# Performance work log

Measured on AMD Instinct MI355X. Metric: run time of the kernel, lower is better.

The kernel has to match this reference:

```python
import jax, jax.numpy as jnp
import numpy as np

V, E, H, S = 50257, 1024, 1024, 2048


def setup_inputs() -> dict:
    key = jax.random.key(0)
    ks = jax.random.split(key, 24)
    def n(k, shape, s=0.02):
        return jax.random.normal(k, shape, dtype=jnp.float32) * s
    inp = {
        "x": jax.random.normal(ks[0], (1, E), dtype=jnp.float32),
        "encoder_outputs": jax.random.normal(ks[1], (S, 2 * H), dtype=jnp.float32),
        "sentence": jax.random.randint(ks[2], (S,), 0, V, dtype=jnp.int32).at[0].set(7),
        "prev_probs": jax.random.uniform(ks[3], (V + S,), dtype=jnp.float32),
        "h0": n(ks[4], (1, H), 1.0),
        "c0": n(ks[5], (1, H), 1.0),
        "attn_W": n(ks[6], (S, 2 * H)), "attn_b": jnp.zeros((S,), jnp.float32),
        "comb_W": n(ks[7], (H, 2 * H)), "comb_b": jnp.zeros((H,), jnp.float32),
        "Ws_W": n(ks[8], (H, 2 * H)), "Ws_b": jnp.zeros((H,), jnp.float32),
        "Wo_W": n(ks[9], (V, H)), "Wo_b": jnp.zeros((V,), jnp.float32),
        "Wc_W": n(ks[10], (H, 2 * H)), "Wc_b": jnp.zeros((H,), jnp.float32),
        "W_ih": n(ks[11], (4 * H, E + 2 * H)), "W_hh": n(ks[12], (4 * H, H)),
        "b_ih": jnp.zeros((4 * H,), jnp.float32), "b_hh": jnp.zeros((4 * H,), jnp.float32),
        "prev_word": 7,
    }
    return inp


def reference(x, encoder_outputs, sentence, prev_probs, h0, c0,
              attn_W, attn_b, comb_W, comb_b, Ws_W, Ws_b,
              Wo_W, Wo_b, Wc_W, Wc_b, W_ih, W_hh, b_ih, b_hh, prev_word):
    xe, h, c = x[0], h0[0], c0[0]            # [E], [H], [H]
    # attentive read: attention over encoder positions, then combine to [H]
    att_logits = jnp.concatenate([xe, h]) @ attn_W.T + attn_b      # [S]
    attn_w = jax.nn.softmax(att_logits)
    ctx = attn_w @ encoder_outputs                                 # [2H]
    attentive = ctx @ comb_W.T + comb_b                            # [H]
    # selective read (copy mechanism): positions where sentence == prev_word
    probs_c = prev_probs[V:]                                       # [S]
    rho = jnp.where(sentence == prev_word, probs_c, 0.0)
    rho = rho / (rho.sum() + 1e-9)
    selective = (rho @ encoder_outputs) @ Ws_W.T + Ws_b            # [H]
    # single LSTM step (PyTorch gate order i,f,g,o)
    lstm_in = jnp.concatenate([xe, selective, attentive])          # [E+2H]
    gates = lstm_in @ W_ih.T + b_ih + h @ W_hh.T + b_hh            # [4H]
    i, f, g, o = jnp.split(gates, 4)
    c1 = jax.nn.sigmoid(f) * c + jax.nn.sigmoid(i) * jnp.tanh(g)
    h1 = jax.nn.sigmoid(o) * jnp.tanh(c1)                          # [H]
    # generate + copy scores, joint softmax
    score_g = h1 @ Wo_W.T + Wo_b                                   # [V]
    score_c = jnp.tanh(encoder_outputs @ Wc_W.T + Wc_b) @ h1       # [S]
    probs = jax.nn.softmax(jnp.concatenate([score_g, score_c]))    # [V+S]
    return probs, h1[None, :], c1[None, :]
```

## Files before the change

### kernel.cpp

```cpp
#include <hip/hip_runtime.h>
#include <hip/hip_bf16.h>
#include <math.h>

#define VV 50257
#define EE 1024
#define HH 1024
#define SS 2048
#define VS (VV + SS)

#define NSCB 2048

#define OFF_LOGA   0
#define OFF_CTX    2048
#define OFF_SEL    4096
#define OFF_LSTMIN 6144
#define OFF_GATES  9216
#define OFF_LOG    13312
#define OFF_MS     65664
#define OFF_LS     67712
#define OFF_T0     69760
#define OFF_T1     (69760 + 2048*1024)
#define OFF_ENCB   (OFF_T1 + 2048*1024)
#define OFF_WCB    (OFF_ENCB + 2048*1024)

typedef __attribute__((ext_vector_type(8))) short bf16x8;
typedef __attribute__((ext_vector_type(8))) unsigned short u16x8;
typedef __attribute__((ext_vector_type(4))) float f32x4;

__device__ inline float wave_reduce(float v) {
    #pragma unroll
    for (int off = 32; off > 0; off >>= 1) v += __shfl_down(v, off, 64);
    return v;
}

__device__ inline unsigned short f2bf(float f) {
    unsigned int u = __builtin_bit_cast(unsigned int, f);
    u += 0x7FFFu + ((u >> 16) & 1u);
    return (unsigned short)(u >> 16);
}

__global__ __launch_bounds__(256) void k_front(
        const float* __restrict__ x, const float* __restrict__ h0,
        const float* __restrict__ attn_W, const float* __restrict__ attn_b,
        float* __restrict__ loga,
        const float* __restrict__ enc, const float* __restrict__ Wc_W,
        unsigned short* __restrict__ encb, unsigned short* __restrict__ Wcb,
        float* __restrict__ ctxsel, float* __restrict__ lstm_in) {
    int bx = blockIdx.x, tid = threadIdx.x;
    if (bx < 512) {
        int wave = (bx * 256 + tid) >> 6;
        int lane = tid & 63;
        const float4* rp = (const float4*)(attn_W + (size_t)wave * 2048);
        float acc = 0.f;
        #pragma unroll
        for (int k = 0; k < 8; ++k) {
            int idx = lane + 64 * k;
            float4 w = rp[idx];
            int j = idx * 4;
            const float* cat = (j < 1024) ? (x + j) : (h0 + (j - 1024));
            acc += w.x * cat[0] + w.y * cat[1] + w.z * cat[2] + w.w * cat[3];
        }
        acc = wave_reduce(acc);
        if (lane == 0) loga[wave] = acc + attn_b[wave];
        return;
    }
    if (bx < 1280) {
        bool isenc = bx < 1024;
        int b = isenc ? bx - 512 : bx - 1024;
        const float* src = isenc ? enc : Wc_W;
        unsigned short* dst = isenc ? encb : Wcb;
        size_t base = (size_t)b * 8192;
        #pragma unroll
        for (int p = 0; p < 8; ++p) {
            size_t idx = base + p * 1024 + tid * 4;
            float4 v = *(const float4*)(src + idx);
            ushort4 o = { f2bf(v.x), f2bf(v.y), f2bf(v.z), f2bf(v.w) };
            *(ushort4*)(dst + idx) = o;
        }
        return;
    }
    if (bx == 1280) {
        for (int j = tid; j < 4096; j += 256) ctxsel[j] = 0.f;
        return;
    }
    for (int j = tid; j < EE; j += 256) lstm_in[j] = x[j];
}

__global__ __launch_bounds__(256) void k_ctx(
        const float* __restrict__ enc, const float* __restrict__ logits,
        const int* __restrict__ sentence, const float* __restrict__ prev_probs,
        const int* __restrict__ prev_word,
        float* __restrict__ ctx, float* __restrict__ selctx) {
    __shared__ float red[256];
    __shared__ float aw[64], rh[64];
    int tid = threadIdx.x;
    float m = -1e30f;
    for (int s = tid; s < SS; s += 256) m = fmaxf(m, logits[s]);
    red[tid] = m; __syncthreads();
    for (int o = 128; o > 0; o >>= 1) { if (tid < o) red[tid] = fmaxf(red[tid], red[tid + o]); __syncthreads(); }
    m = red[0]; __syncthreads();
    float sum = 0.f;
    for (int s = tid; s < SS; s += 256) sum += __expf(logits[s] - m);
    red[tid] = sum; __syncthreads();
    for (int o = 128; o > 0; o >>= 1) { if (tid < o) red[tid] += red[tid + o]; __syncthreads(); }
    float inv = 1.f / red[0]; __syncthreads();
    int pw = prev_word[0];
    float rsum = 0.f;
    for (int s = tid; s < SS; s += 256) rsum += (sentence[s] == pw) ? prev_probs[VV + s] : 0.f;
    red[tid] = rsum; __syncthreads();
    for (int o = 128; o > 0; o >>= 1) { if (tid < o) red[tid] += red[tid + o]; __syncthreads(); }
    float rinv = 1.f / (red[0] + 1e-9f); __syncthreads();
    int s0 = blockIdx.y * 64;
    if (tid < 64) {
        int s = s0 + tid;
        aw[tid] = __expf(logits[s] - m) * inv;
        rh[tid] = ((sentence[s] == pw) ? prev_probs[VV + s] : 0.f) * rinv;
    }
    __syncthreads();
    int col4 = blockIdx.x * 256 + tid;
    float4 a = {0.f, 0.f, 0.f, 0.f}, r = {0.f, 0.f, 0.f, 0.f};
    const float4* p = (const float4*)enc + (size_t)s0 * 512 + col4;
    #pragma unroll 4
    for (int i = 0; i < 64; ++i) {
        float4 v = p[(size_t)i * 512];
        float w = aw[i], q = rh[i];
        a.x += w * v.x; a.y += w * v.y; a.z += w * v.z; a.w += w * v.w;
        r.x += q * v.x; r.y += q * v.y; r.z += q * v.z; r.w += q * v.w;
    }
    int c = col4 * 4;
    atomicAdd(&ctx[c], a.x); atomicAdd(&ctx[c+1], a.y); atomicAdd(&ctx[c+2], a.z); atomicAdd(&ctx[c+3], a.w);
    atomicAdd(&selctx[c], r.x); atomicAdd(&selctx[c+1], r.y); atomicAdd(&selctx[c+2], r.z); atomicAdd(&selctx[c+3], r.w);
}

__global__ __launch_bounds__(256) void k_comb(
        const float* __restrict__ ctx, const float* __restrict__ selctx,
        const float* __restrict__ comb_W, const float* __restrict__ comb_b,
        const float* __restrict__ Ws_W, const float* __restrict__ Ws_b,
        float* __restrict__ lstm_in) {
    int wave = (blockIdx.x * blockDim.x + threadIdx.x) >> 6;
    int lane = threadIdx.x & 63;
    bool sel = wave >= 1024;
    int i = sel ? wave - 1024 : wave;
    const float4* rp = (const float4*)((sel ? Ws_W : comb_W) + (size_t)i * 2048);
    const float4* vp = (const float4*)(sel ? selctx : ctx);
    float acc = 0.f;
    #pragma unroll
    for (int k = 0; k < 8; ++k) {
        int idx = lane + 64 * k;
        float4 w = rp[idx]; float4 v = vp[idx];
        acc += w.x * v.x + w.y * v.y + w.z * v.z + w.w * v.w;
    }
    acc = wave_reduce(acc);
    if (lane == 0) lstm_in[sel ? (1024 + i) : (2048 + i)] = acc + (sel ? Ws_b[i] : comb_b[i]);
}

__global__ __launch_bounds__(256) void k_gates_gemm(
        const float* __restrict__ lstm_in, const float* __restrict__ h0,
        const float* __restrict__ W_ih, const float* __restrict__ W_hh,
        const float* __restrict__ b_ih, const float* __restrict__ b_hh,
        float* __restrict__ gates,
        const unsigned short* __restrict__ Ab,
        const unsigned short* __restrict__ Bb,
        float* __restrict__ T0, float* __restrict__ T1) {
    __shared__ __attribute__((aligned(16))) unsigned short As[128 * 32];
    __shared__ __attribute__((aligned(16))) unsigned short Bs[128 * 32];
    int tid = threadIdx.x;
    if (blockIdx.x < 1024) {
        int wave = (blockIdx.x * 256 + tid) >> 6;
        int lane = tid & 63;
        const float4* rp = (const float4*)(W_ih + (size_t)wave * 3072);
        const float4* vp = (const float4*)lstm_in;
        float acc = 0.f;
        #pragma unroll
        for (int k = 0; k < 12; ++k) {
            int idx = lane + 64 * k;
            float4 w = rp[idx]; float4 v = vp[idx];
            acc += w.x * v.x + w.y * v.y + w.z * v.z + w.w * v.w;
        }
        const float4* hp = (const float4*)(W_hh + (size_t)wave * 1024);
        const float4* h4 = (const float4*)h0;
        #pragma unroll
        for (int k = 0; k < 4; ++k) {
            int idx = lane + 64 * k;
            float4 w = hp[idx]; float4 v = h4[idx];
            acc += w.x * v.x + w.y * v.y + w.z * v.z + w.w * v.w;
        }
        acc = wave_reduce(acc);
        if (lane == 0) gates[wave] = acc + b_ih[wave] + b_hh[wave];
        return;
    }
    int gg = blockIdx.x - 1024;
    int sK = gg >> 7;
    int rem = gg & 127;
    int mbase = (rem >> 3) * 128;
    int nbase = (rem & 7) * 128;
    float* C = sK ? T1 : T0;
    int lane = tid & 63;
    int wid = tid >> 6;
    int wm = (wid >> 1) * 64;
    int wn = (wid & 1) * 64;
    int lrow = lane & 15;
    int lk = (lane >> 4) * 8;
    f32x4 acc[4][4] = {};
    int kbeg = sK * 1024;
    for (int k0 = kbeg; k0 < kbeg + 1024; k0 += 32) {
        #pragma unroll
        for (int p = 0; p < 2; ++p) {
            int fi = p * 256 + tid;
            int row = fi >> 2;
            int c8 = fi & 3;
            *(u16x8*)(As + row * 32 + c8 * 8) =
                *(const u16x8*)(Ab + (size_t)(mbase + row) * 2048 + k0 + c8 * 8);
            *(u16x8*)(Bs + row * 32 + c8 * 8) =
                *(const u16x8*)(Bb + (size_t)(nbase + row) * 2048 + k0 + c8 * 8);
        }
        __syncthreads();
        bf16x8 af[4], bfr[4];
        #pragma unroll
        for (int t = 0; t < 4; ++t) {
            af[t]  = *(const bf16x8*)(As + (wm + t * 16 + lrow) * 32 + lk);
            bfr[t] = *(const bf16x8*)(Bs + (wn + t * 16 + lrow) * 32 + lk);
        }
        #pragma unroll
        for (int mt = 0; mt < 4; ++mt)
            #pragma unroll
            for (int nt = 0; nt < 4; ++nt)
                acc[mt][nt] = __builtin_amdgcn_mfma_f32_16x16x32_bf16(af[mt], bfr[nt], acc[mt][nt], 0, 0, 0);
        __syncthreads();
    }
    int crow0 = (lane >> 4) * 4;
    int ccol = lane & 15;
    #pragma unroll
    for (int mt = 0; mt < 4; ++mt)
        #pragma unroll
        for (int nt = 0; nt < 4; ++nt) {
            int col = nbase + wn + nt * 16 + ccol;
            #pragma unroll
            for (int r = 0; r < 4; ++r) {
                int row = mbase + wm + mt * 16 + crow0 + r;
                C[(size_t)row * 1024 + col] = acc[mt][nt][r];
            }
        }
}

__global__ __launch_bounds__(256) void k_scores(
        const float* __restrict__ gates, const float* __restrict__ c0,
        const float* __restrict__ Wo_W, const float* __restrict__ Wo_b,
        const float* __restrict__ T0, const float* __restrict__ T1,
        const float* __restrict__ Wc_b,
        float* __restrict__ logits, float* __restrict__ out,
        float* __restrict__ ms, float* __restrict__ ls) {
    __shared__ float h1s[1024];
    __shared__ float wm_s[4], wl_s[4];
    int tid = threadIdx.x, bid = blockIdx.x;
    #pragma unroll
    for (int kk = 0; kk < 4; ++kk) {
        int j = tid + 256 * kk;
        float ig = gates[j], fg = gates[1024 + j], gg = gates[2048 + j], og = gates[3072 + j];
        float si = 1.f / (1.f + __expf(-ig));
        float sf = 1.f / (1.f + __expf(-fg));
        float so = 1.f / (1.f + __expf(-og));
        float c1 = sf * c0[j] + si * tanhf(gg);
        float h1 = so * tanhf(c1);
        h1s[j] = h1;
        if (bid == 0) { out[VS + j] = h1; out[VS + 1024 + j] = c1; }
    }
    __syncthreads();
    int lane = tid & 63, wid = tid >> 6;
    int gw = bid * 4 + wid;
    float m = -1e30f, l = 0.f;
    const float4* hp = (const float4*)h1s;
    for (int v = gw; v < VS; v += NSCB * 4) {
        float acc = 0.f;
        if (v < VV) {
            const float4* rp = (const float4*)(Wo_W + (size_t)v * 1024);
            #pragma unroll
            for (int k = 0; k < 4; ++k) {
                int idx = lane + 64 * k;
                float4 w = rp[idx]; float4 hv = hp[idx];
                acc += w.x * hv.x + w.y * hv.y + w.z * hv.z + w.w * hv.w;
            }
        } else {
            int r = v - VV;
            const float4* p0 = (const float4*)(T0 + (size_t)r * 1024);
            const float4* p1 = (const float4*)(T1 + (size_t)r * 1024);
            const float4* bp = (const float4*)Wc_b;
            #pragma unroll
            for (int k = 0; k < 4; ++k) {
                int idx = lane + 64 * k;
                float4 a0 = p0[idx], a1 = p1[idx], bb = bp[idx], hv = hp[idx];
                acc += tanhf(a0.x + a1.x + bb.x) * hv.x + tanhf(a0.y + a1.y + bb.y) * hv.y
                     + tanhf(a0.z + a1.z + bb.z) * hv.z + tanhf(a0.w + a1.w + bb.w) * hv.w;
            }
        }
        acc = wave_reduce(acc);
        if (lane == 0) {
            float lg = acc + (v < VV ? Wo_b[v] : 0.f);
            logits[v] = lg;
            float nm = fmaxf(m, lg);
            l = l * __expf(m - nm) + __expf(lg - nm);
            m = nm;
        }
    }
    if (lane == 0) { wm_s[wid] = m; wl_s[wid] = l; }
    __syncthreads();
    if (tid == 0) {
        float M = wm_s[0], L = wl_s[0];
        #pragma unroll
        for (int w = 1; w < 4; ++w) {
            float nm = fmaxf(M, wm_s[w]);
            L = L * __expf(M - nm) + wl_s[w] * __expf(wm_s[w] - nm);
            M = nm;
        }
        ms[bid] = M; ls[bid] = L;
    }
}

__global__ __launch_bounds__(256) void k_smfinal(
        const float* __restrict__ ms, const float* __restrict__ ls,
        const float* __restrict__ logits, float* __restrict__ out) {
    __shared__ float rm[256], rl[256];
    int tid = threadIdx.x;
    float m = -1e30f, l = 0.f;
    for (int i = tid; i < NSCB; i += 256) {
        float bm = ms[i], bl = ls[i];
        float nm = fmaxf(m, bm);
        l = l * __expf(m - nm) + bl * __expf(bm - nm);
        m = nm;
    }
    rm[tid] = m; rl[tid] = l; __syncthreads();
    for (int o = 128; o > 0; o >>= 1) {
        if (tid < o) {
            float m2 = rm[tid + o], l2 = rl[tid + o];
            float nm = fmaxf(rm[tid], m2);
            rl[tid] = rl[tid] * __expf(rm[tid] - nm) + l2 * __expf(m2 - nm);
            rm[tid] = nm;
        }
        __syncthreads();
    }
    float M = rm[0], Linv = 1.f / rl[0];
    for (int v = blockIdx.x * 256 + tid; v < VS; v += 128 * 256)
        out[v] = __expf(logits[v] - M) * Linv;
}

extern "C" void kernel_launch(void* const* d_in, const int* in_sizes, int n_in,
                              void* d_out, int out_size, void* d_ws, size_t ws_size,
                              hipStream_t stream) {
    (void)in_sizes; (void)n_in; (void)out_size; (void)ws_size;
    const float* x          = (const float*)d_in[0];
    const float* enc        = (const float*)d_in[1];
    const int*   sentence   = (const int*)d_in[2];
    const float* prev_probs = (const float*)d_in[3];
    const float* h0         = (const float*)d_in[4];
    const float* c0         = (const float*)d_in[5];
    const float* attn_W     = (const float*)d_in[6];
    const float* attn_b     = (const float*)d_in[7];
    const float* comb_W     = (const float*)d_in[8];
    const float* comb_b     = (const float*)d_in[9];
    const float* Ws_W       = (const float*)d_in[10];
    const float* Ws_b       = (const float*)d_in[11];
    const float* Wo_W       = (const float*)d_in[12];
    const float* Wo_b       = (const float*)d_in[13];
    const float* Wc_W       = (const float*)d_in[14];
    const float* Wc_b       = (const float*)d_in[15];
    const float* W_ih       = (const float*)d_in[16];
    const float* W_hh       = (const float*)d_in[17];
    const float* b_ih       = (const float*)d_in[18];
    const float* b_hh       = (const float*)d_in[19];
    const int*   prev_word  = (const int*)d_in[20];
    float* ws  = (float*)d_ws;
    float* out = (float*)d_out;
    unsigned short* encb = (unsigned short*)(ws + OFF_ENCB);
    unsigned short* Wcb  = (unsigned short*)(ws + OFF_WCB);

    k_front<<<1282, 256, 0, stream>>>(x, h0, attn_W, attn_b, ws + OFF_LOGA,
                                      enc, Wc_W, encb, Wcb,
                                      ws + OFF_CTX, ws + OFF_LSTMIN);
    k_ctx<<<dim3(2, 32), 256, 0, stream>>>(enc, ws + OFF_LOGA, sentence, prev_probs,
                                           prev_word, ws + OFF_CTX, ws + OFF_SEL);
    k_comb<<<512, 256, 0, stream>>>(ws + OFF_CTX, ws + OFF_SEL, comb_W, comb_b,
                                    Ws_W, Ws_b, ws + OFF_LSTMIN);
    k_gates_gemm<<<1280, 256, 0, stream>>>(ws + OFF_LSTMIN, h0, W_ih, W_hh, b_ih, b_hh,
                                           ws + OFF_GATES, encb, Wcb,
                                           ws + OFF_T0, ws + OFF_T1);
    k_scores<<<NSCB, 256, 0, stream>>>(ws + OFF_GATES, c0, Wo_W, Wo_b,
                                       ws + OFF_T0, ws + OFF_T1, Wc_b,
                                       ws + OFF_LOG, out, ws + OFF_MS, ws + OFF_LS);
    k_smfinal<<<128, 256, 0, stream>>>(ws + OFF_MS, ws + OFF_LS, ws + OFF_LOG, out);
}
```

Before: 451.9 us.

## Fuse copy-score GEMM with tanh and h1 dot into scores kernel epilogue

The encoder×Wc bf16 MFMA GEMM moves out of the gates kernel and into the scores kernel. Its epilogue applies the bias, tanh and the h1 dot product directly on the accumulators and atomically adds the result into a 2048-entry copy-score vector. This removes the two 8 MB fp32 intermediate tensors (split-K halves) that were written and then re-read. The GEMM now uses 256 blocks with 64-row tiles and full K, so per-block work is longer and the GEMM runs alongside the Wo GEMV blocks, which may hurt load balance. The final softmax kernel now folds the copy scores in directly.

```diff
diff --git a/kernel.cpp b/kernel.cpp
--- a/kernel.cpp
+++ b/kernel.cpp
@@ -8,20 +8,20 @@
 #define SS 2048
 #define VS (VV + SS)
 
-#define NSCB 2048
+#define NWOB 1792
+#define NWOW (NWOB * 4)
 
 #define OFF_LOGA   0
 #define OFF_CTX    2048
 #define OFF_SEL    4096
-#define OFF_LSTMIN 6144
-#define OFF_GATES  9216
-#define OFF_LOG    13312
-#define OFF_MS     65664
-#define OFF_LS     67712
-#define OFF_T0     69760
-#define OFF_T1     (69760 + 2048*1024)
-#define OFF_ENCB   (OFF_T1 + 2048*1024)
-#define OFF_WCB    (OFF_ENCB + 2048*1024)
+#define OFF_SCOREC 6144
+#define OFF_LSTMIN 8192
+#define OFF_GATES  11264
+#define OFF_LOG    15360
+#define OFF_MS     67712
+#define OFF_LS     69504
+#define OFF_ENCB   71296
+#define OFF_WCB    (71296 + 2097152)
 
 typedef __attribute__((ext_vector_type(8))) short bf16x8;
 typedef __attribute__((ext_vector_type(8))) unsigned short u16x8;
@@ -45,7 +45,7 @@
         float* __restrict__ loga,
         const float* __restrict__ enc, const float* __restrict__ Wc_W,
         unsigned short* __restrict__ encb, unsigned short* __restrict__ Wcb,
-        float* __restrict__ ctxsel, float* __restrict__ lstm_in) {
+        float* __restrict__ zbase, float* __restrict__ lstm_in) {
     int bx = blockIdx.x, tid = threadIdx.x;
     if (bx < 512) {
         int wave = (bx * 256 + tid) >> 6;
@@ -80,7 +80,7 @@
         return;
     }
     if (bx == 1280) {
-        for (int j = tid; j < 4096; j += 256) ctxsel[j] = 0.f;
+        for (int j = tid; j < 6144; j += 256) zbase[j] = 0.f;
         return;
     }
     for (int j = tid; j < EE; j += 256) lstm_in[j] = x[j];
@@ -118,18 +118,18 @@
     }
     __syncthreads();
     int col4 = blockIdx.x * 256 + tid;
-    float4 a = {0.f, 0.f, 0.f, 0.f}, r = {0.f, 0.f, 0.f, 0.f};
+    float4 a = {0.f,0.f,0.f,0.f}, r = {0.f,0.f,0.f,0.f};
     const float4* p = (const float4*)enc + (size_t)s0 * 512 + col4;
     #pragma unroll 4
     for (int i = 0; i < 64; ++i) {
         float4 v = p[(size_t)i * 512];
         float w = aw[i], q = rh[i];
-        a.x += w * v.x; a.y += w * v.y; a.z += w * v.z; a.w += w * v.w;
-        r.x += q * v.x; r.y += q * v.y; r.z += q * v.z; r.w += q * v.w;
+        a.x += w*v.x; a.y += w*v.y; a.z += w*v.z; a.w += w*v.w;
+        r.x += q*v.x; r.y += q*v.y; r.z += q*v.z; r.w += q*v.w;
     }
     int c = col4 * 4;
-    atomicAdd(&ctx[c], a.x); atomicAdd(&ctx[c+1], a.y); atomicAdd(&ctx[c+2], a.z); atomicAdd(&ctx[c+3], a.w);
-    atomicAdd(&selctx[c], r.x); atomicAdd(&selctx[c+1], r.y); atomicAdd(&selctx[c+2], r.z); atomicAdd(&selctx[c+3], r.w);
+    atomicAdd(&ctx[c],   a.x); atomicAdd(&ctx[c+1],   a.y); atomicAdd(&ctx[c+2],   a.z); atomicAdd(&ctx[c+3],   a.w);
+    atomicAdd(&selctx[c],r.x); atomicAdd(&selctx[c+1],r.y); atomicAdd(&selctx[c+2],r.z); atomicAdd(&selctx[c+3],r.w);
 }
 
 __global__ __launch_bounds__(256) void k_comb(
@@ -148,111 +148,55 @@
     for (int k = 0; k < 8; ++k) {
         int idx = lane + 64 * k;
         float4 w = rp[idx]; float4 v = vp[idx];
-        acc += w.x * v.x + w.y * v.y + w.z * v.z + w.w * v.w;
+        acc += w.x*v.x + w.y*v.y + w.z*v.z + w.w*v.w;
     }
     acc = wave_reduce(acc);
     if (lane == 0) lstm_in[sel ? (1024 + i) : (2048 + i)] = acc + (sel ? Ws_b[i] : comb_b[i]);
 }
 
-__global__ __launch_bounds__(256) void k_gates_gemm(
+__global__ __launch_bounds__(256) void k_gates(
         const float* __restrict__ lstm_in, const float* __restrict__ h0,
         const float* __restrict__ W_ih, const float* __restrict__ W_hh,
         const float* __restrict__ b_ih, const float* __restrict__ b_hh,
-        float* __restrict__ gates,
-        const unsigned short* __restrict__ Ab,
-        const unsigned short* __restrict__ Bb,
-        float* __restrict__ T0, float* __restrict__ T1) {
-    __shared__ __attribute__((aligned(16))) unsigned short As[128 * 32];
-    __shared__ __attribute__((aligned(16))) unsigned short Bs[128 * 32];
-    int tid = threadIdx.x;
-    if (blockIdx.x < 1024) {
-        int wave = (blockIdx.x * 256 + tid) >> 6;
-        int lane = tid & 63;
-        const float4* rp = (const float4*)(W_ih + (size_t)wave * 3072);
-        const float4* vp = (const float4*)lstm_in;
-        float acc = 0.f;
-        #pragma unroll
-        for (int k = 0; k < 12; ++k) {
-            int idx = lane + 64 * k;
-            float4 w = rp[idx]; float4 v = vp[idx];
-            acc += w.x * v.x + w.y * v.y + w.z * v.z + w.w * v.w;
-        }
-        const float4* hp = (const float4*)(W_hh + (size_t)wave * 1024);
-        const float4* h4 = (const float4*)h0;
-        #pragma unroll
-        for (int k = 0; k < 4; ++k) {
-            int idx = lane + 64 * k;
-            float4 w = hp[idx]; float4 v = h4[idx];
-            acc += w.x * v.x + w.y * v.y + w.z * v.z + w.w * v.w;
-        }
-        acc = wave_reduce(acc);
-        if (lane == 0) gates[wave] = acc + b_ih[wave] + b_hh[wave];
-        return;
-    }
-    int gg = blockIdx.x - 1024;
-    int sK = gg >> 7;
-    int rem = gg & 127;
-    int mbase = (rem >> 3) * 128;
-    int nbase = (rem & 7) * 128;
-    float* C = sK ? T1 : T0;
-    int lane = tid & 63;
-    int wid = tid >> 6;
-    int wm = (wid >> 1) * 64;
-    int wn = (wid & 1) * 64;
-    int lrow = lane & 15;
-    int lk = (lane >> 4) * 8;
-    f32x4 acc[4][4] = {};
-    int kbeg = sK * 1024;
-    for (int k0 = kbeg; k0 < kbeg + 1024; k0 += 32) {
-        #pragma unroll
-        for (int p = 0; p < 2; ++p) {
-            int fi = p * 256 + tid;
-            int row = fi >> 2;
-            int c8 = fi & 3;
-            *(u16x8*)(As + row * 32 + c8 * 8) =
-                *(const u16x8*)(Ab + (size_t)(mbase + row) * 2048 + k0 + c8 * 8);
-            *(u16x8*)(Bs + row * 32 + c8 * 8) =
-                *(const u16x8*)(Bb + (size_t)(nbase + row) * 2048 + k0 + c8 * 8);
-        }
-        __syncthreads();
-        bf16x8 af[4], bfr[4];
-        #pragma unroll
-        for (int t = 0; t < 4; ++t) {
-            af[t]  = *(const bf16x8*)(As + (wm + t * 16 + lrow) * 32 + lk);
-            bfr[t] = *(const bf16x8*)(Bs + (wn + t * 16 + lrow) * 32 + lk);
-        }
-        #pragma unroll
-        for (int mt = 0; mt < 4; ++mt)
-            #pragma unroll
-            for (int nt = 0; nt < 4; ++nt)
-                acc[mt][nt] = __builtin_amdgcn_mfma_f32_16x16x32_bf16(af[mt], bfr[nt], acc[mt][nt], 0, 0, 0);
-        __syncthreads();
-    }
-    int crow0 = (lane >> 4) * 4;
-    int ccol = lane & 15;
-    #pragma unroll
-    for (int mt = 0; mt < 4; ++mt)
-        #pragma unroll
-        for (int nt = 0; nt < 4; ++nt) {
-            int col = nbase + wn + nt * 16 + ccol;
-            #pragma unroll
-            for (int r = 0; r < 4; ++r) {
-                int row = mbase + wm + mt * 16 + crow0 + r;
-                C[(size_t)row * 1024 + col] = acc[mt][nt][r];
-            }
-        }
+        float* __restrict__ gates) {
+    int wave = (blockIdx.x * 256 + threadIdx.x) >> 6;
+    int lane = threadIdx.x & 63;
+    const float4* rp = (const float4*)(W_ih + (size_t)wave * 3072);
+    const float4* vp = (const float4*)lstm_in;
+    float acc = 0.f;
+    #pragma unroll
+    for (int k = 0; k < 12; ++k) {
+        int idx = lane + 64 * k;
+        float4 w = rp[idx]; float4 v = vp[idx];
+        acc += w.x*v.x + w.y*v.y + w.z*v.z + w.w*v.w;
+    }
+    const float4* hp = (const float4*)(W_hh + (size_t)wave * 1024);
+    const float4* h4 = (const float4*)h0;
+    #pragma unroll
+    for (int k = 0; k < 4; ++k) {
+        int idx = lane + 64 * k;
+        float4 w = hp[idx]; float4 v = h4[idx];
+        acc += w.x*v.x + w.y*v.y + w.z*v.z + w.w*v.w;
+    }
+    acc = wave_reduce(acc);
+    if (lane == 0) gates[wave] = acc + b_ih[wave] + b_hh[wave];
 }
 
 __global__ __launch_bounds__(256) void k_scores(
         const float* __restrict__ gates, const float* __restrict__ c0,
         const float* __restrict__ Wo_W, const float* __restrict__ Wo_b,
-        const float* __restrict__ T0, const float* __restrict__ T1,
         const float* __restrict__ Wc_b,
+        const unsigned short* __restrict__ encb, const unsigned short* __restrict__ Wcb,
         float* __restrict__ logits, float* __restrict__ out,
-        float* __restrict__ ms, float* __restrict__ ls) {
+        float* __restrict__ ms, float* __restrict__ ls,
+        float* __restrict__ scorec) {
+    __shared__ __attribute__((aligned(16))) unsigned short As[64 * 32];
+    __shared__ __attribute__((aligned(16))) unsigned short Bs[128 * 32];
     __shared__ float h1s[1024];
     __shared__ float wm_s[4], wl_s[4];
     int tid = threadIdx.x, bid = blockIdx.x;
+    int lane = tid & 63, wid = tid >> 6;
+
     #pragma unroll
     for (int kk = 0; kk < 4; ++kk) {
         int j = tid + 256 * kk;
@@ -266,36 +210,85 @@
         if (bid == 0) { out[VS + j] = h1; out[VS + 1024 + j] = c1; }
     }
     __syncthreads();
-    int lane = tid & 63, wid = tid >> 6;
-    int gw = bid * 4 + wid;
+
+    if (bid < 256) {
+        int mbase = (bid >> 3) * 64;
+        int nbase = (bid & 7) * 128;
+        int wm = (wid >> 1) * 32;
+        int wn = (wid & 1) * 64;
+        int lrow = lane & 15;
+        int lk = (lane >> 4) * 8;
+        f32x4 acc[2][4] = {};
+        for (int k0 = 0; k0 < 2048; k0 += 32) {
+            {
+                int row = tid >> 2, c8 = tid & 3;
+                *(u16x8*)(As + row * 32 + c8 * 8) =
+                    *(const u16x8*)(encb + (size_t)(mbase + row) * 2048 + k0 + c8 * 8);
+            }
+            #pragma unroll
+            for (int p = 0; p < 2; ++p) {
+                int fi = p * 256 + tid;
+                int row = fi >> 2, c8 = fi & 3;
+                *(u16x8*)(Bs + row * 32 + c8 * 8) =
+                    *(const u16x8*)(Wcb + (size_t)(nbase + row) * 2048 + k0 + c8 * 8);
+            }
+            __syncthreads();
+            bf16x8 af[2], bfr[4];
+            #pragma unroll
+            for (int t = 0; t < 2; ++t)
+                af[t] = *(const bf16x8*)(As + (wm + t * 16 + lrow) * 32 + lk);
+            #pragma unroll
+            for (int t = 0; t < 4; ++t)
+                bfr[t] = *(const bf16x8*)(Bs + (wn + t * 16 + lrow) * 32 + lk);
+            #pragma unroll
+            for (int mt = 0; mt < 2; ++mt)
+                #pragma unroll
+                for (int nt = 0; nt < 4; ++nt)
+                    acc[mt][nt] = __builtin_amdgcn_mfma_f32_16x16x32_bf16(af[mt], bfr[nt], acc[mt][nt], 0, 0, 0);
+            __syncthreads();
+        }
+        int ccol = lane & 15;
+        float bc[4], hc[4];
+        #pragma unroll
+        for (int nt = 0; nt < 4; ++nt) {
+            int col = nbase + wn + nt * 16 + ccol;
+            bc[nt] = Wc_b[col];
+            hc[nt] = h1s[col];
+        }
+        #pragma unroll
+        for (int mt = 0; mt < 2; ++mt)
+            #pragma unroll
+            for (int r = 0; r < 4; ++r) {
+                float p = 0.f;
+                #pragma unroll
+                for (int nt = 0; nt < 4; ++nt)
+                    p += tanhf(acc[mt][nt][r] + bc[nt]) * hc[nt];
+                #pragma unroll
+                for (int off = 1; off < 16; off <<= 1) p += __shfl_xor(p, off, 64);
+                if ((lane & 15) == 0) {
+                    int row = mbase + wm + mt * 16 + (lane >> 4) * 4 + r;
+                    atomicAdd(&scorec[row], p);
+                }
+            }
+        return;
+    }
+
+    int wb = bid - 256;
+    int gw = wb * 4 + wid;
     float m = -1e30f, l = 0.f;
     const float4* hp = (const float4*)h1s;
-    for (int v = gw; v < VS; v += NSCB * 4) {
+    for (int v = gw; v < VV; v += NWOW) {
+        const float4* rp = (const float4*)(Wo_W + (size_t)v * 1024);
         float acc = 0.f;
-        if (v < VV) {
-            const float4* rp = (const float4*)(Wo_W + (size_t)v * 1024);
-            #pragma unroll
-            for (int k = 0; k < 4; ++k) {
-                int idx = lane + 64 * k;
-                float4 w = rp[idx]; float4 hv = hp[idx];
-                acc += w.x * hv.x + w.y * hv.y + w.z * hv.z + w.w * hv.w;
-            }
-        } else {
-            int r = v - VV;
-            const float4* p0 = (const float4*)(T0 + (size_t)r * 1024);
-            const float4* p1 = (const float4*)(T1 + (size_t)r * 1024);
-            const float4* bp = (const float4*)Wc_b;
-            #pragma unroll
-            for (int k = 0; k < 4; ++k) {
-                int idx = lane + 64 * k;
-                float4 a0 = p0[idx], a1 = p1[idx], bb = bp[idx], hv = hp[idx];
-                acc += tanhf(a0.x + a1.x + bb.x) * hv.x + tanhf(a0.y + a1.y + bb.y) * hv.y
-                     + tanhf(a0.z + a1.z + bb.z) * hv.z + tanhf(a0.w + a1.w + bb.w) * hv.w;
-            }
+        #pragma unroll
+        for (int k = 0; k < 4; ++k) {
+            int idx = lane + 64 * k;
+            float4 w = rp[idx]; float4 hv = hp[idx];
+            acc += w.x*hv.x + w.y*hv.y + w.z*hv.z + w.w*hv.w;
         }
         acc = wave_reduce(acc);
         if (lane == 0) {
-            float lg = acc + (v < VV ? Wo_b[v] : 0.f);
+            float lg = acc + Wo_b[v];
             logits[v] = lg;
             float nm = fmaxf(m, lg);
             l = l * __expf(m - nm) + __expf(lg - nm);
@@ -312,20 +305,27 @@
             L = L * __expf(M - nm) + wl_s[w] * __expf(wm_s[w] - nm);
             M = nm;
         }
-        ms[bid] = M; ls[bid] = L;
-    }
-}
-
-__global__ __launch_bounds__(256) void k_smfinal(
+        ms[wb] = M; ls[wb] = L;
+    }
+}
+
+__global__ __launch_bounds__(256) void k_final(
         const float* __restrict__ ms, const float* __restrict__ ls,
-        const float* __restrict__ logits, float* __restrict__ out) {
+        const float* __restrict__ scorec, const float* __restrict__ logits,
+        float* __restrict__ out) {
     __shared__ float rm[256], rl[256];
     int tid = threadIdx.x;
     float m = -1e30f, l = 0.f;
-    for (int i = tid; i < NSCB; i += 256) {
+    for (int i = tid; i < NWOB; i += 256) {
         float bm = ms[i], bl = ls[i];
         float nm = fmaxf(m, bm);
         l = l * __expf(m - nm) + bl * __expf(bm - nm);
+        m = nm;
+    }
+    for (int i = tid; i < SS; i += 256) {
+        float x = scorec[i];
+        float nm = fmaxf(m, x);
+        l = l * __expf(m - nm) + __expf(x - nm);
         m = nm;
     }
     rm[tid] = m; rl[tid] = l; __syncthreads();
@@ -339,8 +339,10 @@
         __syncthreads();
     }
     float M = rm[0], Linv = 1.f / rl[0];
-    for (int v = blockIdx.x * 256 + tid; v < VS; v += 128 * 256)
-        out[v] = __expf(logits[v] - M) * Linv;
+    for (int v = blockIdx.x * 256 + tid; v < VS; v += 128 * 256) {
+        float lg = (v < VV) ? logits[v] : scorec[v - VV];
+        out[v] = __expf(lg - M) * Linv;
+    }
 }
 
 extern "C" void kernel_launch(void* const* d_in, const int* in_sizes, int n_in,
@@ -380,11 +382,11 @@
                                            prev_word, ws + OFF_CTX, ws + OFF_SEL);
     k_comb<<<512, 256, 0, stream>>>(ws + OFF_CTX, ws + OFF_SEL, comb_W, comb_b,
                                     Ws_W, Ws_b, ws + OFF_LSTMIN);
-    k_gates_gemm<<<1280, 256, 0, stream>>>(ws + OFF_LSTMIN, h0, W_ih, W_hh, b_ih, b_hh,
-                                           ws + OFF_GATES, encb, Wcb,
-                                           ws + OFF_T0, ws + OFF_T1);
-    k_scores<<<NSCB, 256, 0, stream>>>(ws + OFF_GATES, c0, Wo_W, Wo_b,
-                                       ws + OFF_T0, ws + OFF_T1, Wc_b,
-                                       ws + OFF_LOG, out, ws + OFF_MS, ws + OFF_LS);
-    k_smfinal<<<128, 256, 0, stream>>>(ws + OFF_MS, ws + OFF_LS, ws + OFF_LOG, out);
-}
+    k_gates<<<1024, 256, 0, stream>>>(ws + OFF_LSTMIN, h0, W_ih, W_hh, b_ih, b_hh,
+                                      ws + OFF_GATES);
+    k_scores<<<2048, 256, 0, stream>>>(ws + OFF_GATES, c0, Wo_W, Wo_b, Wc_b,
+                                       encb, Wcb, ws + OFF_LOG, out,
+                                       ws + OFF_MS, ws + OFF_LS, ws + OFF_SCOREC);
+    k_final<<<128, 256, 0, stream>>>(ws + OFF_MS, ws + OFF_LS, ws + OFF_SCOREC,
+                                     ws + OFF_LOG, out);
+}
```

Result: no change. 446.1 us (-1.3%).
